# Kernel tuning notes

Measured on AMD Instinct MI355X. Metric: run time of the kernel, lower is better.

The kernel has to match this reference:

```python
import math
import jax, jax.numpy as jnp
import numpy as np

EMBED_DIM = 512
NUM_CLASSES = 100000
BATCH = 1024
SCALE = 64.0
MARGIN = 0.5
EASY_MARGIN = False

COS_M = math.cos(MARGIN)
SIN_M = math.sin(MARGIN)
TH = math.cos(math.pi - MARGIN)
MM = math.sin(math.pi - MARGIN) * MARGIN


def setup_inputs() -> dict:
    key = jax.random.key(0)
    k1, k2, k3 = jax.random.split(key, 3)
    embeddings = jax.random.normal(k1, (BATCH, EMBED_DIM), dtype=jnp.float32)
    labels = jax.random.randint(k2, (BATCH,), 0, NUM_CLASSES, dtype=jnp.int64)
    # xavier_uniform over (num_classes, embedding_dim)
    limit = math.sqrt(6.0 / (NUM_CLASSES + EMBED_DIM))
    weight = jax.random.uniform(k3, (NUM_CLASSES, EMBED_DIM), dtype=jnp.float32,
                                minval=-limit, maxval=limit)
    return {"embeddings": embeddings, "labels": labels, "weight": weight}


def _l2norm(x, eps=1e-12):
    # matches torch F.normalize(p=2): x / max(||x||, eps)
    n = jnp.sqrt(jnp.sum(x * x, axis=1, keepdims=True))
    return x / jnp.maximum(n, eps)


def reference(embeddings, labels, weight):
    emb = _l2norm(embeddings)            # (B, D)
    w = _l2norm(weight)                  # (C, D)
    cos_theta = emb @ w.T                # (B, C)
    cos_theta = jnp.clip(cos_theta, -1.0 + 1e-07, 1.0 - 1e-07)
    sin_theta = jnp.sqrt(1.0 - cos_theta * cos_theta)
    cos_theta_m = cos_theta * COS_M - sin_theta * SIN_M
    if EASY_MARGIN:
        cos_theta_m = jnp.where(cos_theta > 0, cos_theta_m, cos_theta)
    else:
        cos_theta_m = jnp.where(cos_theta > TH, cos_theta_m, cos_theta - MM)
    # one-hot blend: margin applied only at target column per row
    one_hot = (jnp.arange(NUM_CLASSES)[None, :] == labels[:, None])  # (B, C) bool
    logits = jnp.where(one_hot, cos_theta_m, cos_theta) * SCALE
    return logits
```

## Files before the change

### kernel.cpp

```cpp
#include <hip/hip_runtime.h>
#include <hip/hip_bf16.h>

#define NCLS   100000
#define NPAD   100096
#define BATCH  1024
#define EDIM   512

#define COS_M_  0.8775825618903728f
#define SIN_M_  0.479425538604203f
#define TH_     (-0.8775825618903728f)
#define MM_     0.2397127693021015f
#define SCALE_  64.0f

typedef __attribute__((ext_vector_type(8))) short short8;
typedef __attribute__((ext_vector_type(4))) float f32x4;

__device__ __forceinline__ ushort f2bf(float f) {
    uint u = __float_as_uint(f);
    u += 0x7fffu + ((u >> 16) & 1u);
    return (ushort)(u >> 16);
}

__global__ __launch_bounds__(256) void norm_rows_kernel(
    const float* __restrict__ in, ushort* __restrict__ out,
    int rows, int padrows)
{
    int gw   = (int)((blockIdx.x * blockDim.x + threadIdx.x) >> 6);
    int lane = (int)(threadIdx.x & 63);
    if (gw >= padrows) return;
    ushort* op = out + (size_t)gw * EDIM + lane * 8;
    if (gw >= rows) {
        uint4 z = make_uint4(0u, 0u, 0u, 0u);
        *(uint4*)op = z;
        return;
    }
    const float* ip = in + (size_t)gw * EDIM + lane * 8;
    float4 x0 = *(const float4*)ip;
    float4 x1 = *(const float4*)(ip + 4);
    float ss = x0.x*x0.x + x0.y*x0.y + x0.z*x0.z + x0.w*x0.w
             + x1.x*x1.x + x1.y*x1.y + x1.z*x1.z + x1.w*x1.w;
    #pragma unroll
    for (int off = 32; off; off >>= 1) ss += __shfl_xor(ss, off, 64);
    float inv = 1.0f / fmaxf(sqrtf(ss), 1e-12f);
    uint w0 = (uint)f2bf(x0.x*inv) | ((uint)f2bf(x0.y*inv) << 16);
    uint w1 = (uint)f2bf(x0.z*inv) | ((uint)f2bf(x0.w*inv) << 16);
    uint w2 = (uint)f2bf(x1.x*inv) | ((uint)f2bf(x1.y*inv) << 16);
    uint w3 = (uint)f2bf(x1.z*inv) | ((uint)f2bf(x1.w*inv) << 16);
    uint4 r; r.x = w0; r.y = w1; r.z = w2; r.w = w3;
    *(uint4*)op = r;
}

__global__ __launch_bounds__(256) void fixup_labels_kernel(
    const int* __restrict__ labels, float* __restrict__ C)
{
    int row = (int)(blockIdx.x * blockDim.x + threadIdx.x);
    if (row >= BATCH) return;
    int lab = labels[row];
    float* p = C + (size_t)row * NCLS + lab;
    float c = *p * (1.0f / SCALE_);
    float s  = sqrtf(1.0f - c * c);
    float cm = c * COS_M_ - s * SIN_M_;
    cm = (c > TH_) ? cm : (c - MM_);
    *p = cm * SCALE_;
}

#define GLL16(g, s) __builtin_amdgcn_global_load_lds(                    \
    (const __attribute__((address_space(1))) void*)(g),                  \
    (__attribute__((address_space(3))) void*)(s), 16, 0, 0)

__global__ __launch_bounds__(256, 3) void gemm_arc_kernel(
    const ushort* __restrict__ A,
    const ushort* __restrict__ B,
    float* __restrict__ C)
{
    __shared__ __align__(16) ushort Als[3][128 * 32];
    __shared__ __align__(16) ushort Bls[3][128 * 32];

    const int t    = (int)threadIdx.x;
    const int lane = t & 63;
    const int w    = t >> 6;
    const int wrow = w >> 1, wcol = w & 1;
    const int lr   = lane & 15, lg = lane >> 4;

    const int nwg  = (int)gridDim.x;
    const int cpx  = nwg >> 3;
    const int bid  = (int)blockIdx.x;
    const int swz  = (bid & 7) * cpx + (bid >> 3);
    const int brow = swz & 7;
    const int bcol = swz >> 3;

    const f32x4 z4 = {0.f, 0.f, 0.f, 0.f};
    f32x4 acc[4][4];
    #pragma unroll
    for (int i = 0; i < 4; ++i)
        #pragma unroll
        for (int j = 0; j < 4; ++j) acc[i][j] = z4;

    const int srow = t >> 2;
    const int scb  = ((t & 3) * 16) ^ (((t >> 3) & 3) << 4);
    const char* Ab = (const char*)(A + ((size_t)brow * 128 + srow) * EDIM) + scb;
    const char* Bb = (const char*)(B + ((size_t)bcol * 128 + srow) * EDIM) + scb;
    const uint ldsw = (uint)w * 1024;

    const int kswz  = ((lr >> 1) & 3) << 4;
    const int aoff0 = (wrow * 64 + lr) * 64 + ((lg * 16) ^ kswz);
    const int boff0 = (wcol * 64 + lr) * 64 + ((lg * 16) ^ kswz);

#define STAGE(c, kt) do {                                                  \
        const char* a0 = Ab + (kt) * 64;                                   \
        const char* b0 = Bb + (kt) * 64;                                   \
        char* Ad = (char*)Als + (size_t)(c) * 8192 + ldsw;                 \
        char* Bd = (char*)Bls + (size_t)(c) * 8192 + ldsw;                 \
        GLL16(a0,                 Ad);                                     \
        GLL16(a0 + 64 * EDIM * 2, Ad + 4096);                              \
        GLL16(b0,                 Bd);                                     \
        GLL16(b0 + 64 * EDIM * 2, Bd + 4096);                              \
    } while (0)

#define COMPUTE(c) do {                                                    \
        const char* Ap = (const char*)Als + (size_t)(c) * 8192;            \
        const char* Bp = (const char*)Bls + (size_t)(c) * 8192;            \
        short8 av[4], bv[4];                                               \
        _Pragma("unroll")                                                  \
        for (int mi = 0; mi < 4; ++mi)                                     \
            av[mi] = *(const short8*)(Ap + aoff0 + mi * 1024);             \
        _Pragma("unroll")                                                  \
        for (int ni = 0; ni < 4; ++ni)                                     \
            bv[ni] = *(const short8*)(Bp + boff0 + ni * 1024);             \
        _Pragma("unroll")                                                  \
        for (int mi = 0; mi < 4; ++mi)                                     \
            _Pragma("unroll")                                              \
            for (int ni = 0; ni < 4; ++ni)                                 \
                acc[mi][ni] = __builtin_amdgcn_mfma_f32_16x16x32_bf16(     \
                    bv[ni], av[mi], acc[mi][ni], 0, 0, 0);                 \
    } while (0)

    STAGE(0, 0);
    STAGE(1, 1);

    #pragma unroll
    for (int kt = 0; kt < 14; ++kt) {
        asm volatile("s_waitcnt lgkmcnt(0)" ::: "memory");
        __builtin_amdgcn_s_barrier();
        STAGE((kt + 2) % 3, kt + 2);
        asm volatile("s_waitcnt vmcnt(8)" ::: "memory");
        __builtin_amdgcn_s_barrier();
        COMPUTE(kt % 3);
    }
    asm volatile("s_waitcnt vmcnt(4)" ::: "memory");
    __builtin_amdgcn_s_barrier();
    COMPUTE(14 % 3);
    asm volatile("s_waitcnt vmcnt(0)" ::: "memory");
    __builtin_amdgcn_s_barrier();
    COMPUTE(15 % 3);

    const int mbase = brow * 128 + wrow * 64;
    const int nbase = bcol * 128 + wcol * 64;
    #pragma unroll
    for (int mi = 0; mi < 4; ++mi) {
        const int grow = mbase + mi * 16 + lr;
        float* crow = C + (size_t)grow * NCLS;
        #pragma unroll
        for (int ni = 0; ni < 4; ++ni) {
            if (nbase + ni * 16 < NCLS) {
                f32x4 v = acc[mi][ni];
                f32x4 o;
                #pragma unroll
                for (int j = 0; j < 4; ++j) {
                    float cc = fminf(fmaxf(v[j], -1.0f + 1e-7f), 1.0f - 1e-7f);
                    o[j] = cc * SCALE_;
                }
                __builtin_nontemporal_store(o,
                    (f32x4*)&crow[nbase + ni * 16 + lg * 4]);
            }
        }
    }
#undef STAGE
#undef COMPUTE
}

extern "C" void kernel_launch(void* const* d_in, const int* in_sizes, int n_in,
                              void* d_out, int out_size, void* d_ws, size_t ws_size,
                              hipStream_t stream)
{
    const float* emb    = (const float*)d_in[0];
    const int*   labels = (const int*)d_in[1];
    const float* wgt    = (const float*)d_in[2];
    float*       out    = (float*)d_out;

    ushort* Ebf = (ushort*)d_ws;
    ushort* Wbf = (ushort*)((char*)d_ws + (size_t)BATCH * EDIM * 2);

    norm_rows_kernel<<<BATCH / 4, 256, 0, stream>>>(emb, Ebf, BATCH, BATCH);
    norm_rows_kernel<<<NPAD / 4, 256, 0, stream>>>(wgt, Wbf, NCLS, NPAD);

    gemm_arc_kernel<<<(BATCH / 128) * (NPAD / 128), 256, 0, stream>>>(Ebf, Wbf, out);

    fixup_labels_kernel<<<BATCH / 256, 256, 0, stream>>>(labels, out);
}
```

Before: 223.6 us.

## Merge normalization launches and switch GEMM to double-buffered LDS for occupancy

The two row-normalization launches are merged into one kernel that handles embedding and weight rows by global warp index, removing a launch. The GEMM's LDS pipeline goes from three stages to two, which cuts shared memory per block. The launch bound rises from 3 to 4 blocks per CU, trading prefetch depth for more resident waves to hide memory latency. The kernel is largely bound by writing the output, so the effect may be small.

```diff
diff --git a/kernel.cpp b/kernel.cpp
--- a/kernel.cpp
+++ b/kernel.cpp
@@ -21,20 +21,28 @@
     return (ushort)(u >> 16);
 }
 
-__global__ __launch_bounds__(256) void norm_rows_kernel(
-    const float* __restrict__ in, ushort* __restrict__ out,
-    int rows, int padrows)
+__global__ __launch_bounds__(256) void norm_all_kernel(
+    const float* __restrict__ emb, const float* __restrict__ wgt,
+    ushort* __restrict__ Ebf, ushort* __restrict__ Wbf)
 {
     int gw   = (int)((blockIdx.x * blockDim.x + threadIdx.x) >> 6);
     int lane = (int)(threadIdx.x & 63);
-    if (gw >= padrows) return;
-    ushort* op = out + (size_t)gw * EDIM + lane * 8;
-    if (gw >= rows) {
-        uint4 z = make_uint4(0u, 0u, 0u, 0u);
-        *(uint4*)op = z;
-        return;
+    const float* ip;
+    ushort* op;
+    if (gw < BATCH) {
+        ip = emb + (size_t)gw * EDIM + lane * 8;
+        op = Ebf + (size_t)gw * EDIM + lane * 8;
+    } else {
+        int wr = gw - BATCH;
+        if (wr >= NPAD) return;
+        op = Wbf + (size_t)wr * EDIM + lane * 8;
+        if (wr >= NCLS) {
+            uint4 z = make_uint4(0u, 0u, 0u, 0u);
+            *(uint4*)op = z;
+            return;
+        }
+        ip = wgt + (size_t)wr * EDIM + lane * 8;
     }
-    const float* ip = in + (size_t)gw * EDIM + lane * 8;
     float4 x0 = *(const float4*)ip;
     float4 x1 = *(const float4*)(ip + 4);
     float ss = x0.x*x0.x + x0.y*x0.y + x0.z*x0.z + x0.w*x0.w
@@ -68,13 +76,13 @@
     (const __attribute__((address_space(1))) void*)(g),                  \
     (__attribute__((address_space(3))) void*)(s), 16, 0, 0)
 
-__global__ __launch_bounds__(256, 3) void gemm_arc_kernel(
+__global__ __launch_bounds__(256, 4) void gemm_arc_kernel(
     const ushort* __restrict__ A,
     const ushort* __restrict__ B,
     float* __restrict__ C)
 {
-    __shared__ __align__(16) ushort Als[3][128 * 32];
-    __shared__ __align__(16) ushort Bls[3][128 * 32];
+    __shared__ __align__(16) ushort Als[2][128 * 32];
+    __shared__ __align__(16) ushort Bls[2][128 * 32];
 
     const int t    = (int)threadIdx.x;
     const int lane = t & 63;
@@ -136,23 +144,19 @@
     } while (0)
 
     STAGE(0, 0);
-    STAGE(1, 1);
-
-    #pragma unroll
-    for (int kt = 0; kt < 14; ++kt) {
+
+    #pragma unroll
+    for (int kt = 0; kt < 15; ++kt) {
         asm volatile("s_waitcnt lgkmcnt(0)" ::: "memory");
         __builtin_amdgcn_s_barrier();
-        STAGE((kt + 2) % 3, kt + 2);
-        asm volatile("s_waitcnt vmcnt(8)" ::: "memory");
+        STAGE((kt + 1) & 1, kt + 1);
+        asm volatile("s_waitcnt vmcnt(4)" ::: "memory");
         __builtin_amdgcn_s_barrier();
-        COMPUTE(kt % 3);
+        COMPUTE(kt & 1);
     }
-    asm volatile("s_waitcnt vmcnt(4)" ::: "memory");
-    __builtin_amdgcn_s_barrier();
-    COMPUTE(14 % 3);
     asm volatile("s_waitcnt vmcnt(0)" ::: "memory");
     __builtin_amdgcn_s_barrier();
-    COMPUTE(15 % 3);
+    COMPUTE(15 & 1);
 
     const int mbase = brow * 128 + wrow * 64;
     const int nbase = bcol * 128 + wcol * 64;
@@ -191,8 +195,7 @@
     ushort* Ebf = (ushort*)d_ws;
     ushort* Wbf = (ushort*)((char*)d_ws + (size_t)BATCH * EDIM * 2);
 
-    norm_rows_kernel<<<BATCH / 4, 256, 0, stream>>>(emb, Ebf, BATCH, BATCH);
-    norm_rows_kernel<<<NPAD / 4, 256, 0, stream>>>(wgt, Wbf, NCLS, NPAD);
+    norm_all_kernel<<<(BATCH + NPAD) / 4, 256, 0, stream>>>(emb, wgt, Ebf, Wbf);
 
     gemm_arc_kernel<<<(BATCH / 128) * (NPAD / 128), 256, 0, stream>>>(Ebf, Wbf, out);
 
```

Result: no change. 221.6 us (-0.9%).
